# Optimization experiments

Measured on AMD Instinct MI355X. Metric: run time of the kernel, lower is better.

Reference implementation:

```python
import jax, jax.numpy as jnp
import numpy as np

B, N, M, C, T, HF, WF = 4, 512, 32, 512, 8, 14, 14
K = 80          # num_classes
P = 7           # ROI pool output size
HID = 1024
IMG = 224


def setup_inputs() -> dict:
    key = jax.random.key(0)
    k0, k1, k2, k3, k4, k5 = jax.random.split(key, 6)
    feature = jax.random.normal(k0, (B, C, T, HF, WF), dtype=jnp.float32)
    # GT boxes: realistic xyxy boxes inside a 224x224 image
    ka, kb = jax.random.split(k1)
    cxy = jax.random.uniform(ka, (B, M, 2), minval=40.0, maxval=180.0)
    wh = jax.random.uniform(kb, (B, M, 2), minval=40.0, maxval=100.0)
    gt_bboxes = jnp.concatenate([cxy - wh / 2, cxy + wh / 2], axis=-1).astype(jnp.float32)
    # Proposals: jittered copies of GT boxes so many pass the IoU>=0.85 fg test
    idx = jnp.arange(N) % M
    base = gt_bboxes[:, idx]                                   # [B,N,4]
    noise = jax.random.normal(k2, (B, N, 4), dtype=jnp.float32) * 1.5
    proposal_bboxes = jnp.clip(base + noise, 0.0, float(IMG))
    gt_classes = (jax.random.uniform(k3, (B, M, K)) < 0.1).astype(jnp.float32)
    W1 = jax.random.normal(k4, (C * P * P, HID), dtype=jnp.float32) * 0.01
    b1 = jnp.zeros((HID,), jnp.float32)
    W2 = jax.random.normal(k5, (HID, K), dtype=jnp.float32) * 0.01
    b2 = jnp.zeros((K,), jnp.float32)
    return {"feature": feature, "proposal_bboxes": proposal_bboxes,
            "gt_bboxes": gt_bboxes, "gt_classes": gt_classes,
            "W1": W1, "b1": b1, "W2": W2, "b2": b2,
            "image_h": IMG, "image_w": IMG}


def _iou(a, b):
    # a [B,N,4], b [B,M,4] xyxy -> [B,N,M]
    lt = jnp.maximum(a[:, :, None, :2], b[:, None, :, :2])
    rb = jnp.minimum(a[:, :, None, 2:], b[:, None, :, 2:])
    wh = jnp.clip(rb - lt, 0.0)
    inter = wh[..., 0] * wh[..., 1]
    area_a = (a[..., 2] - a[..., 0]) * (a[..., 3] - a[..., 1])
    area_b = (b[..., 2] - b[..., 0]) * (b[..., 3] - b[..., 1])
    return inter / (area_a[:, :, None] + area_b[:, None, :] - inter + 1e-8)


def _roi_pool(feat_bhwc, boxes, bidx, sy, sx):
    # feat_bhwc [B,H,W,C]; boxes [R,4] image coords; bilinear 7x7 ROI pooling
    H, W = feat_bhwc.shape[1], feat_bhwc.shape[2]
    x1, y1, x2, y2 = boxes[:, 0] * sx, boxes[:, 1] * sy, boxes[:, 2] * sx, boxes[:, 3] * sy
    g = (jnp.arange(P, dtype=jnp.float32) + 0.5) / P
    ys = y1[:, None] + g[None, :] * (y2 - y1)[:, None]        # [R,P]
    xs = x1[:, None] + g[None, :] * (x2 - x1)[:, None]        # [R,P]
    y = jnp.broadcast_to(ys[:, :, None], (boxes.shape[0], P, P)) - 0.5
    x = jnp.broadcast_to(xs[:, None, :], (boxes.shape[0], P, P)) - 0.5
    y0f = jnp.floor(y); x0f = jnp.floor(x)
    wy = jnp.clip(y - y0f, 0.0, 1.0)[..., None]
    wx = jnp.clip(x - x0f, 0.0, 1.0)[..., None]
    y0 = jnp.clip(y0f, 0, H - 1).astype(jnp.int32)
    y1i = jnp.clip(y0f + 1, 0, H - 1).astype(jnp.int32)
    x0 = jnp.clip(x0f, 0, W - 1).astype(jnp.int32)
    x1i = jnp.clip(x0f + 1, 0, W - 1).astype(jnp.int32)
    bi = bidx[:, None, None]
    gather = lambda yy, xx: feat_bhwc[bi, yy, xx]             # [R,P,P,C]
    out = (gather(y0, x0) * (1 - wy) * (1 - wx) + gather(y0, x1i) * (1 - wy) * wx +
           gather(y1i, x0) * wy * (1 - wx) + gather(y1i, x1i) * wy * wx)
    return out


def reference(feature, proposal_bboxes, gt_bboxes, gt_classes, W1, b1, W2, b2, image_h, image_w):
    # temporal average pool (AvgPool3d over T) -> [B,C,HF,WF]
    feat = feature.mean(axis=2)
    feat_bhwc = jnp.transpose(feat, (0, 2, 3, 1))             # [B,HF,WF,C]
    # IoU-based fg assignment
    ious = _iou(proposal_bboxes, gt_bboxes)                   # [B,N,M]
    max_iou = ious.max(axis=2)                                # [B,N]
    assign = ious.argmax(axis=2)                              # [B,N]
    any_fg = jnp.any(max_iou >= 0.85)
    thresh = jnp.where(any_fg, 0.85, 0.5)                     # fallback branch
    fg = (max_iou >= thresh).astype(feature.dtype)            # [B,N]
    # ROI pool all proposals (bg masked out in the loss)
    boxes = proposal_bboxes.reshape(B * N, 4)
    bidx = jnp.repeat(jnp.arange(B, dtype=jnp.int32), N)
    sy = feat.shape[2] / float(image_h)
    sx = feat.shape[3] / float(image_w)
    pool = _roi_pool(feat_bhwc, boxes, bidx, sy, sx)          # [R,P,P,C]
    pool = jnp.transpose(pool, (0, 3, 1, 2)).reshape(B * N, C * P * P)
    hidden = jax.nn.relu(pool @ W1 + b1)                      # [R,HID]
    logits = hidden @ W2 + b2                                 # [R,K]
    # multilabel soft-margin labels per proposal
    labels = gt_classes[jnp.repeat(jnp.arange(B), N), assign.reshape(-1)]  # [R,K]
    per = -(labels * jax.nn.log_sigmoid(logits) +
            (1.0 - labels) * jax.nn.log_sigmoid(-logits)).mean(axis=-1)    # [R]
    per = per.reshape(B, N)
    cnt = fg.sum(axis=1)
    losses = jnp.where(cnt > 0, (per * fg).sum(axis=1) / jnp.maximum(cnt, 1.0), 0.0)
    return losses
```

## Files before the change

kernel.cpp:

```cpp
#include <hip/hip_runtime.h>
#include <cstdint>
#include <cstddef>

#define KTOT 25088
#define NBOX 2048
#define HID  1024

typedef __bf16 bf16x8 __attribute__((ext_vector_type(8)));
typedef float  f32x4  __attribute__((ext_vector_type(4)));

__device__ __forceinline__ unsigned short f2bf(float f) {
  union { float f; unsigned u; } v; v.f = f;
  unsigned r = v.u + 0x7FFFu + ((v.u >> 16) & 1u);
  return (unsigned short)(r >> 16);
}

__device__ __forceinline__ float scalar_f(const void* p) {
  int iv = *(const int*)p;
  if (iv > 0 && iv < (1 << 20)) return (float)iv;
  return *(const float*)p;
}

__global__ __launch_bounds__(256) void k_meant(const float* __restrict__ feature,
                                               float* __restrict__ fbhwc) {
  int id = blockIdx.x * 256 + threadIdx.x;
  if (id >= 4 * 512 * 196) return;
  int pix = id % 196;
  int c   = (id / 196) & 511;
  int b   = id / (196 * 512);
  const float* p = feature + ((size_t)(b * 512 + c) * 8) * 196 + pix;
  float s = 0.f;
#pragma unroll
  for (int t = 0; t < 8; ++t) s += p[t * 196];
  fbhwc[((size_t)(b * 196 + pix)) * 512 + c] = s * 0.125f;
}

__global__ __launch_bounds__(256) void k_iou(const float* __restrict__ prop,
                                             const float* __restrict__ gtb,
                                             float* __restrict__ max_iou,
                                             int* __restrict__ assign,
                                             int* __restrict__ flag) {
  __shared__ float g[128];
  int gid = blockIdx.x * 256 + threadIdx.x;
  int b = gid >> 9;
  if (threadIdx.x < 128) g[threadIdx.x] = gtb[b * 128 + threadIdx.x];
  __syncthreads();
  float x1 = prop[gid * 4 + 0], y1 = prop[gid * 4 + 1];
  float x2 = prop[gid * 4 + 2], y2 = prop[gid * 4 + 3];
  float aa = (x2 - x1) * (y2 - y1);
  float best = -1e30f; int arg = 0;
  for (int m = 0; m < 32; ++m) {
    float gx1 = g[m*4], gy1 = g[m*4+1], gx2 = g[m*4+2], gy2 = g[m*4+3];
    float iw = fmaxf(fminf(x2, gx2) - fmaxf(x1, gx1), 0.f);
    float ih = fmaxf(fminf(y2, gy2) - fmaxf(y1, gy1), 0.f);
    float inter = iw * ih;
    float ab = (gx2 - gx1) * (gy2 - gy1);
    float iou = inter / (aa + ab - inter + 1e-8f);
    if (iou > best) { best = iou; arg = m; }
  }
  max_iou[gid] = best; assign[gid] = arg;
  if (best >= 0.85f) atomicOr(flag, 1);
}

__global__ __launch_bounds__(256) void k_w1t(const float* __restrict__ W1,
                                             unsigned short* __restrict__ W1T) {
  __shared__ unsigned short tile[64][68];
  int kp0 = blockIdx.x * 64;
  int h0  = blockIdx.y * 64;
  int t = threadIdx.x;
  int seg = t & 15, ro = t >> 4;
#pragma unroll
  for (int r = 0; r < 4; ++r) {
    int i = ro + r * 16;
    int kp = kp0 + i;
    int srow = (kp & 511) * 49 + (kp >> 9);
    float4 v = *(const float4*)(W1 + (size_t)srow * 1024 + h0 + seg * 4);
    tile[i][seg*4+0] = f2bf(v.x);
    tile[i][seg*4+1] = f2bf(v.y);
    tile[i][seg*4+2] = f2bf(v.z);
    tile[i][seg*4+3] = f2bf(v.w);
  }
  __syncthreads();
#pragma unroll
  for (int r = 0; r < 4; ++r) {
    int hi = ro + r * 16;
    unsigned a = tile[seg*4+0][hi];
    unsigned b = tile[seg*4+1][hi];
    unsigned c = tile[seg*4+2][hi];
    unsigned d = tile[seg*4+3][hi];
    *(uint2*)(W1T + (size_t)(h0+hi)*KTOT + kp0 + seg*4) =
        make_uint2(a | (b << 16), c | (d << 16));
  }
}

__global__ __launch_bounds__(256) void k_roipool(const float* __restrict__ fbhwc,
                                                 const float* __restrict__ prop,
                                                 const void* ihp, const void* iwp,
                                                 unsigned short* __restrict__ Apool) {
  int n = blockIdx.x;
  int tid = threadIdx.x;
  float sy = 14.f / scalar_f(ihp);
  float sx = 14.f / scalar_f(iwp);
  float bx1 = prop[n*4+0]*sx, by1 = prop[n*4+1]*sy;
  float bx2 = prop[n*4+2]*sx, by2 = prop[n*4+3]*sy;
  const float* fb = fbhwc + (size_t)(n >> 9) * 196 * 512;
  unsigned short* arow = Apool + (size_t)n * KTOT;
  int c4 = (tid & 127) << 2;
  int bh = tid >> 7;
  for (int b2i = 0; b2i < 49; b2i += 2) {
    int bin = b2i + bh;
    if (bin >= 49) continue;
    int py = bin / 7, px = bin - py * 7;
    float y = by1 + ((py + 0.5f) * (1.f/7.f)) * (by2 - by1) - 0.5f;
    float x = bx1 + ((px + 0.5f) * (1.f/7.f)) * (bx2 - bx1) - 0.5f;
    float y0f = floorf(y), x0f = floorf(x);
    float wy = y - y0f, wx = x - x0f;
    int y0  = min(max((int)y0f, 0), 13);
    int y1i = min(max((int)y0f + 1, 0), 13);
    int x0  = min(max((int)x0f, 0), 13);
    int x1i = min(max((int)x0f + 1, 0), 13);
    float w00 = (1.f - wy) * (1.f - wx), w01 = (1.f - wy) * wx;
    float w10 = wy * (1.f - wx),         w11 = wy * wx;
    const float4 f00 = *(const float4*)(fb + (y0 * 14 + x0 ) * 512 + c4);
    const float4 f01 = *(const float4*)(fb + (y0 * 14 + x1i) * 512 + c4);
    const float4 f10 = *(const float4*)(fb + (y1i * 14 + x0 ) * 512 + c4);
    const float4 f11 = *(const float4*)(fb + (y1i * 14 + x1i) * 512 + c4);
    float vx = f00.x*w00 + f01.x*w01 + f10.x*w10 + f11.x*w11;
    float vy = f00.y*w00 + f01.y*w01 + f10.y*w10 + f11.y*w11;
    float vz = f00.z*w00 + f01.z*w01 + f10.z*w10 + f11.z*w11;
    float vw = f00.w*w00 + f01.w*w01 + f10.w*w10 + f11.w*w11;
    unsigned lo = (unsigned)f2bf(vx) | ((unsigned)f2bf(vy) << 16);
    unsigned hi = (unsigned)f2bf(vz) | ((unsigned)f2bf(vw) << 16);
    *(uint2*)(arow + bin * 512 + c4) = make_uint2(lo, hi);
  }
}

__device__ __forceinline__ void gload16(const unsigned short* g, unsigned short* l) {
  __builtin_amdgcn_global_load_lds(
      (const __attribute__((address_space(1))) unsigned int*)g,
      (__attribute__((address_space(3))) unsigned int*)l, 16, 0, 0);
}

__global__ __launch_bounds__(512, 2) void k_gemm1(
    const unsigned short* __restrict__ A,
    const unsigned short* __restrict__ B,
    unsigned short* __restrict__ hp)
{
  extern __shared__ unsigned short lds[];
  const int tid  = threadIdx.x;
  const int w    = tid >> 6;
  const int lane = tid & 63;
  const int l15  = lane & 15;
  const int wr = w >> 2, wc = w & 3;
  const int bid = (int)blockIdx.x;
  const int wg  = (bid & 7) * 32 + (bid >> 3);
  const int kb  = wg >> 5;
  const int gy  = (wg >> 2) & 7;
  const int gx  = wg & 3;

  f32x4 acc[8][4];
  const f32x4 zero = {0.f, 0.f, 0.f, 0.f};
#pragma unroll
  for (int m = 0; m < 8; ++m)
#pragma unroll
    for (int n = 0; n < 4; ++n) acc[m][n] = zero;

  const int xsw  = (tid & 7) ^ ((tid >> 3) & 7);
  const int rloc = ((tid >> 3) << 1) + (xsw >> 2);
  const int qsrc = xsw & 3;
  const size_t kbase = (size_t)kb * 3136;
  const unsigned short* gAp = A + (size_t)(gy * 256 + rloc) * KTOT + kbase + qsrc * 8;
  const unsigned short* gBp = B + (size_t)(gx * 256 + rloc) * KTOT + kbase + qsrc * 8;
  const int dstc = tid * 8;

  const int pfr   = ((lane >> 4) | ((l15 & 1) << 2)) ^ (l15 >> 1);
  const int aoffc = wr * 4096 + (l15 >> 1) * 64 + pfr * 8;
  const int boffc = wc * 2048 + (l15 >> 1) * 64 + pfr * 8;

  bf16x8 af[4], bfr[4];

#define STGA(OB, KN) { \
    gload16(gAp + (KN),                      lds + (OB) + dstc); \
    gload16(gAp + (KN) + (size_t)128 * KTOT, lds + (OB) + 4096 + dstc); }
#define STGB(OB, KN) { \
    gload16(gBp + (KN),                      lds + (OB) + 8192 + dstc); \
    gload16(gBp + (KN) + (size_t)128 * KTOT, lds + (OB) + 12288 + dstc); }
#define DSRA(CB, MB) _Pragma("unroll") for (int i = 0; i < 4; ++i) \
    af[i] = *reinterpret_cast<const bf16x8*>(lds + (CB) + aoffc + ((MB) + i) * 512);
#define DSRB(CB) _Pragma("unroll") for (int n = 0; n < 4; ++n) \
    bfr[n] = *reinterpret_cast<const bf16x8*>(lds + (CB) + 8192 + boffc + n * 512);
#define MMQ(MH) _Pragma("unroll") for (int i = 0; i < 4; ++i) \
    _Pragma("unroll") for (int n = 0; n < 4; ++n) \
      acc[(MH)*4 + i][n] = __builtin_amdgcn_mfma_f32_16x16x32_bf16( \
          af[i], bfr[n], acc[(MH)*4 + i][n], 0, 0, 0);
#define PHX \
    __builtin_amdgcn_sched_barrier(0); \
    __builtin_amdgcn_s_barrier(); \
    asm volatile("s_waitcnt lgkmcnt(0)" ::: "memory"); \
    __builtin_amdgcn_sched_barrier(0); \
    __builtin_amdgcn_s_setprio(1);
#define VM4 asm volatile("s_waitcnt vmcnt(4)" ::: "memory");
#define VM0 asm volatile("s_waitcnt vmcnt(0)" ::: "memory");
#define VMN

#define KSTEP(CB, OB, KN, DOST, VME)                                          \
  {                                                   \
    DSRA(CB, 0)                                                               \
    DSRB(CB)                                                                  \
    if (DOST) STGA(OB, KN)                                                    \
    PHX  MMQ(0)                                                               \
    __builtin_amdgcn_s_setprio(0);                                            \
    __builtin_amdgcn_s_barrier();                                             \
                        \
    DSRA(CB, 4)                                                               \
    DSRB(CB)                                                                  \
    if (DOST) STGB(OB, KN)                                                    \
    PHX  MMQ(1)                                                               \
    __builtin_amdgcn_s_setprio(0);                                            \
    VME                                                                       \
    __builtin_amdgcn_s_barrier();                                             \
  }

  STGA(0, 0)      STGB(0, 0)
  STGA(16384, 32) STGB(16384, 32)
  VM4
  __builtin_amdgcn_s_barrier();

#pragma unroll 1
  for (int sq = 0; sq < 96; sq += 4) {
    const int kn = (sq + 2) * 32;
    KSTEP(0,     32768, kn,      true, VM4)
    KSTEP(16384, 49152, kn + 32, true, VM4)
    KSTEP(32768, 0,     kn + 64, true, VM4)
    KSTEP(49152, 16384, kn + 96, true, VM4)
  }
  KSTEP(0,     0, 0, false, VM0)
  KSTEP(16384, 0, 0, false, VMN)

#undef KSTEP
#undef VMN
#undef VM0
#undef VM4
#undef PHX
#undef MMQ
#undef DSRB
#undef DSRA
#undef STGB
#undef STGA

  unsigned short* o = hp + (size_t)kb * (2048u * 1024u);
  const int r0 = gy * 256 + wr * 128 + ((lane >> 4) << 2);
  const int c0 = gx * 256 + wc * 64 + l15;
#pragma unroll
  for (int m = 0; m < 8; ++m)
#pragma unroll
    for (int n = 0; n < 4; ++n)
#pragma unroll
      for (int j = 0; j < 4; ++j)
        o[(size_t)(r0 + m * 16 + j) * 1024 + c0 + n * 16] = f2bf(acc[m][n][j]);
}

template<int OUTBF>
__global__ __launch_bounds__(256, 4) void k_gemm(
    const unsigned short* __restrict__ A,
    const unsigned short* __restrict__ B,
    void* __restrict__ outp,
    int Kst, int kIters, int nTileBits, int mTileBits, int ldc)
{
  __shared__ unsigned short As[2][4096];
  __shared__ unsigned short Bs[2][4096];
  const int tid  = threadIdx.x;
  const int w    = tid >> 6;
  const int lane = tid & 63;
  const int nwg = (int)gridDim.x, cpx = nwg >> 3;
  const int bid = (int)blockIdx.x;
  const int wg  = (bid & 7) * cpx + (bid >> 3);
  const int kb  = wg >> (mTileBits + nTileBits);
  const int rem = wg & ((1 << (mTileBits + nTileBits)) - 1);
  const int gy  = rem >> nTileBits;
  const int gx  = rem & ((1 << nTileBits) - 1);
  const int wr = w >> 1, wc = w & 1;

  f32x4 acc[4][4];
  const f32x4 zero = {0.f, 0.f, 0.f, 0.f};
#pragma unroll
  for (int m = 0; m < 4; ++m)
#pragma unroll
    for (int n = 0; n < 4; ++n) acc[m][n] = zero;

  const int r0   = 32 * w + (lane >> 2);
  const int qsrc = (lane & 3) ^ ((lane >> 3) & 3);
  const size_t kbase = (size_t)kb * kIters * 32;
  const unsigned short* gA = A + (size_t)(gy * 128 + r0) * Kst + kbase + qsrc * 8;
  const unsigned short* gB = B + (size_t)(gx * 128 + r0) * Kst + kbase + qsrc * 8;
  const int ldst = r0 * 32 + (lane & 3) * 8;

  const int swq = ((lane >> 4) ^ ((lane >> 1) & 3)) * 8;
  const int ar = (wr * 64 + (lane & 15)) * 32 + swq;
  const int br = (wc * 64 + (lane & 15)) * 32 + swq;

#define STAGE(bufi, it) do {                                         \
    const unsigned short* pa = gA + (size_t)(it) * 32;               \
    const unsigned short* pb = gB + (size_t)(it) * 32;               \
    gload16(pa,                      &As[bufi][ldst]);               \
    gload16(pa + (size_t)16 * Kst,   &As[bufi][ldst + 512]);         \
    gload16(pb,                      &Bs[bufi][ldst]);               \
    gload16(pb + (size_t)16 * Kst,   &Bs[bufi][ldst + 512]);         \
  } while (0)

  STAGE(0, 0);
  int cur = 0;
  for (int kk = 0; kk < kIters; ++kk) {
    __syncthreads();
    if (kk + 1 < kIters) STAGE(cur ^ 1, kk + 1);
    bf16x8 af[4], bfr[4];
#pragma unroll
    for (int m = 0; m < 4; ++m)
      af[m] = *reinterpret_cast<const bf16x8*>(&As[cur][ar + m * 512]);
#pragma unroll
    for (int n = 0; n < 4; ++n)
      bfr[n] = *reinterpret_cast<const bf16x8*>(&Bs[cur][br + n * 512]);
#pragma unroll
    for (int m = 0; m < 4; ++m)
#pragma unroll
      for (int n = 0; n < 4; ++n)
        acc[m][n] = __builtin_amdgcn_mfma_f32_16x16x32_bf16(af[m], bfr[n], acc[m][n], 0, 0, 0);
    cur ^= 1;
  }
#undef STAGE

  const size_t M = (size_t)(1 << mTileBits) * 128;
  const size_t splitStride = M * (size_t)ldc;
  const int r0o = gy * 128 + wr * 64 + ((lane >> 4) << 2);
  const int c0o = gx * 128 + wc * 64 + (lane & 15);
  if (OUTBF) {
    unsigned short* o = (unsigned short*)outp + (size_t)kb * splitStride;
#pragma unroll
    for (int m = 0; m < 4; ++m)
#pragma unroll
      for (int n = 0; n < 4; ++n)
#pragma unroll
        for (int j = 0; j < 4; ++j)
          o[(size_t)(r0o + m * 16 + j) * ldc + c0o + n * 16] = f2bf(acc[m][n][j]);
  } else {
    float* o = (float*)outp + (size_t)kb * splitStride;
#pragma unroll
    for (int m = 0; m < 4; ++m)
#pragma unroll
      for (int n = 0; n < 4; ++n)
#pragma unroll
        for (int j = 0; j < 4; ++j)
          o[(size_t)(r0o + m * 16 + j) * ldc + c0o + n * 16] = acc[m][n][j];
  }
}

__global__ __launch_bounds__(256) void k_combine(const unsigned short* __restrict__ hp,
                                                 const float* __restrict__ b1,
                                                 unsigned short* __restrict__ hidden) {
  int gid = blockIdx.x * 256 + threadIdx.x;
  int id8 = gid * 8;
  int h = id8 & 1023;
  float a[8];
#pragma unroll
  for (int j = 0; j < 8; ++j) a[j] = b1[h + j];
#pragma unroll
  for (int s = 0; s < 8; ++s) {
    uint4 u = *(const uint4*)(hp + (size_t)s * 2097152 + id8);
    unsigned uu[4] = {u.x, u.y, u.z, u.w};
#pragma unroll
    for (int q = 0; q < 4; ++q) {
      union { unsigned u; float f; } lo, hi;
      lo.u = uu[q] << 16; hi.u = uu[q] & 0xFFFF0000u;
      a[2*q]   += lo.f;
      a[2*q+1] += hi.f;
    }
  }
  unsigned out[4];
#pragma unroll
  for (int q = 0; q < 4; ++q) {
    unsigned l  = f2bf(fmaxf(a[2*q],   0.f));
    unsigned hh = f2bf(fmaxf(a[2*q+1], 0.f));
    out[q] = l | (hh << 16);
  }
  *(uint4*)(hidden + id8) = make_uint4(out[0], out[1], out[2], out[3]);
}

__global__ __launch_bounds__(256) void k_w2t(const float* __restrict__ W2,
                                             unsigned short* __restrict__ W2T) {
  int id = blockIdx.x * 256 + threadIdx.x;
  int cls = id >> 10, k = id & 1023;
  float v = (cls < 80) ? W2[(size_t)k * 80 + cls] : 0.f;
  W2T[id] = f2bf(v);
}

__global__ __launch_bounds__(256) void k_bce(const float* __restrict__ hp2,
                                             const float* __restrict__ b2,
                                             const float* __restrict__ gtc,
                                             const int* __restrict__ assign,
                                             float* __restrict__ per) {
  __shared__ float red[256];
  int t = threadIdx.x;
  int box = t >> 4, li = t & 15;
  int n = blockIdx.x * 16 + box;
  int lab = ((n >> 9) * 32 + assign[n]) * 80;
  float s = 0.f;
#pragma unroll
  for (int j = 0; j < 5; ++j) {
    int c = li + 16 * j;
    size_t o = (size_t)n * 128 + c;
    float x = hp2[o] + hp2[o + 262144] + hp2[o + 524288] + hp2[o + 786432] + b2[c];
    float y = gtc[lab + c];
    float ce = log1pf(expf(-fabsf(x)));
    s += y * (fmaxf(-x, 0.f) + ce) + (1.f - y) * (fmaxf(x, 0.f) + ce);
  }
  red[t] = s;
  __syncthreads();
  if (li == 0) {
    float tot = 0.f;
#pragma unroll
    for (int i = 0; i < 16; ++i) tot += red[box * 16 + i];
    per[n] = tot * (1.f / 80.f);
  }
}

__global__ __launch_bounds__(512) void k_reduce(const float* __restrict__ per,
                                                const float* __restrict__ max_iou,
                                                const int* __restrict__ flag,
                                                float* __restrict__ out) {
  __shared__ float sv[8], sf[8];
  int b = blockIdx.x, tid = threadIdx.x;
  float thr = (*flag) ? 0.85f : 0.5f;
  int n = b * 512 + tid;
  float f = (max_iou[n] >= thr) ? 1.f : 0.f;
  float v = per[n] * f;
#pragma unroll
  for (int o = 32; o > 0; o >>= 1) {
    v += __shfl_down(v, o);
    f += __shfl_down(f, o);
  }
  int wv = tid >> 6;
  if ((tid & 63) == 0) { sv[wv] = v; sf[wv] = f; }
  __syncthreads();
  if (tid == 0) {
    float S = 0.f, F = 0.f;
#pragma unroll
    for (int i = 0; i < 8; ++i) { S += sv[i]; F += sf[i]; }
    out[b] = (F > 0.f) ? S / fmaxf(F, 1.f) : 0.f;
  }
}

extern "C" void kernel_launch(void* const* d_in, const int* in_sizes, int n_in,
                              void* d_out, int out_size, void* d_ws, size_t ws_size,
                              hipStream_t stream) {
  const float* feature = (const float*)d_in[0];
  const float* prop    = (const float*)d_in[1];
  const float* gtb     = (const float*)d_in[2];
  const float* gtc     = (const float*)d_in[3];
  const float* W1      = (const float*)d_in[4];
  const float* b1      = (const float*)d_in[5];
  const float* W2      = (const float*)d_in[6];
  const float* b2      = (const float*)d_in[7];
  const void*  ihp     = d_in[8];
  const void*  iwp     = d_in[9];

  char* ws = (char*)d_ws;
  float*          fbhwc  = (float*)(ws);
  unsigned short* W1T    = (unsigned short*)(ws + 1605632);
  unsigned short* Apool  = (unsigned short*)(ws + 52985856);
  unsigned short* hp     = (unsigned short*)(ws + 155746304);
  float*          max_iou= (float*)(ws + 189300736);
  int*            assign = (int*)(ws + 189308928);
  float*          per    = (float*)(ws + 189317120);
  int*            flag   = (int*)(ws + 189325312);
  unsigned short* hidden = W1T;
  unsigned short* W2T    = Apool;
  float*          hp2    = (float*)((char*)Apool + 262144);

  hipFuncSetAttribute((const void*)k_gemm1,
                      hipFuncAttributeMaxDynamicSharedMemorySize, 131072);

  hipMemsetAsync(flag, 0, sizeof(int), stream);
  k_meant  <<<1568, 256, 0, stream>>>(feature, fbhwc);
  k_iou    <<<8, 256, 0, stream>>>(prop, gtb, max_iou, assign, flag);
  k_w1t    <<<dim3(392, 16), 256, 0, stream>>>(W1, W1T);
  k_roipool<<<2048, 256, 0, stream>>>(fbhwc, prop, ihp, iwp, Apool);
  k_gemm1  <<<256, 512, 131072, stream>>>(Apool, W1T, hp);
  k_combine<<<1024, 256, 0, stream>>>(hp, b1, hidden);
  k_w2t    <<<512, 256, 0, stream>>>(W2, W2T);
  k_gemm<0><<<64, 256, 0, stream>>>(hidden, W2T, hp2, 1024, 8, 0, 4, 128);
  k_bce    <<<128, 256, 0, stream>>>(hp2, b2, gtc, assign, per);
  k_reduce <<<4, 512, 0, stream>>>(per, max_iou, flag, (float*)d_out);
}
```

Before: 203.0 us.

## Prefetch next-slot LDS fragments during MFMAs with single barrier per k-step

Restructures the split-K GEMM main loop so that all 8 A fragments and 4 B fragments for the next k-slot are loaded from LDS and interleaved with the current slot's 32 MFMAs. Each k-step now has one barrier instead of two half-steps, each of which needed two barriers. The goal is to hide LDS read latency behind matrix math and cut synchronisation. In exchange the A/B fragment registers roughly double, which adds register pressure, and it relies on the 4-slot ring keeping the next slot ready before its fragments are read.

```diff
diff --git a/kernel.cpp b/kernel.cpp
--- a/kernel.cpp
+++ b/kernel.cpp
@@ -177,76 +177,67 @@
   const int aoffc = wr * 4096 + (l15 >> 1) * 64 + pfr * 8;
   const int boffc = wc * 2048 + (l15 >> 1) * 64 + pfr * 8;
 
-  bf16x8 af[4], bfr[4];
-
-#define STGA(OB, KN) { \
-    gload16(gAp + (KN),                      lds + (OB) + dstc); \
-    gload16(gAp + (KN) + (size_t)128 * KTOT, lds + (OB) + 4096 + dstc); }
-#define STGB(OB, KN) { \
-    gload16(gBp + (KN),                      lds + (OB) + 8192 + dstc); \
-    gload16(gBp + (KN) + (size_t)128 * KTOT, lds + (OB) + 12288 + dstc); }
-#define DSRA(CB, MB) _Pragma("unroll") for (int i = 0; i < 4; ++i) \
-    af[i] = *reinterpret_cast<const bf16x8*>(lds + (CB) + aoffc + ((MB) + i) * 512);
-#define DSRB(CB) _Pragma("unroll") for (int n = 0; n < 4; ++n) \
-    bfr[n] = *reinterpret_cast<const bf16x8*>(lds + (CB) + 8192 + boffc + n * 512);
-#define MMQ(MH) _Pragma("unroll") for (int i = 0; i < 4; ++i) \
-    _Pragma("unroll") for (int n = 0; n < 4; ++n) \
-      acc[(MH)*4 + i][n] = __builtin_amdgcn_mfma_f32_16x16x32_bf16( \
-          af[i], bfr[n], acc[(MH)*4 + i][n], 0, 0, 0);
-#define PHX \
-    __builtin_amdgcn_sched_barrier(0); \
-    __builtin_amdgcn_s_barrier(); \
-    asm volatile("s_waitcnt lgkmcnt(0)" ::: "memory"); \
-    __builtin_amdgcn_sched_barrier(0); \
-    __builtin_amdgcn_s_setprio(1);
+  bf16x8 Afr[8], Bfr[4];
+
+#define STG(SLOT, KN) { \
+    gload16(gAp + (KN),                      lds + (SLOT)*16384 + dstc); \
+    gload16(gAp + (KN) + (size_t)128 * KTOT, lds + (SLOT)*16384 + 4096 + dstc); \
+    gload16(gBp + (KN),                      lds + (SLOT)*16384 + 8192 + dstc); \
+    gload16(gBp + (KN) + (size_t)128 * KTOT, lds + (SLOT)*16384 + 12288 + dstc); }
+#define LDA(i, SLOT) Afr[i] = *reinterpret_cast<const bf16x8*>( \
+    lds + (SLOT)*16384 + aoffc + (i)*512);
+#define LDB(n, SLOT) Bfr[n] = *reinterpret_cast<const bf16x8*>( \
+    lds + (SLOT)*16384 + 8192 + boffc + (n)*512);
 #define VM4 asm volatile("s_waitcnt vmcnt(4)" ::: "memory");
 #define VM0 asm volatile("s_waitcnt vmcnt(0)" ::: "memory");
 #define VMN
 
-#define KSTEP(CB, OB, KN, DOST, VME)                                          \
-  {                                                   \
-    DSRA(CB, 0)                                                               \
-    DSRB(CB)                                                                  \
-    if (DOST) STGA(OB, KN)                                                    \
-    PHX  MMQ(0)                                                               \
-    __builtin_amdgcn_s_setprio(0);                                            \
-    __builtin_amdgcn_s_barrier();                                             \
-                        \
-    DSRA(CB, 4)                                                               \
-    DSRB(CB)                                                                  \
-    if (DOST) STGB(OB, KN)                                                    \
-    PHX  MMQ(1)                                                               \
-    __builtin_amdgcn_s_setprio(0);                                            \
-    VME                                                                       \
-    __builtin_amdgcn_s_barrier();                                             \
-  }
-
-  STGA(0, 0)      STGB(0, 0)
-  STGA(16384, 32) STGB(16384, 32)
+#define STEP(CS, DOSTG, KN, VMASM, DOREFILL)                                   \
+  {                                                                            \
+    if (DOSTG) STG((((CS)+2)&3), KN)                                           \
+    VMASM                                                                      \
+    __builtin_amdgcn_s_barrier();                                              \
+    asm volatile("s_waitcnt lgkmcnt(0)" ::: "memory");                         \
+    __builtin_amdgcn_sched_barrier(0);                                         \
+    __builtin_amdgcn_s_setprio(1);                                             \
+    _Pragma("unroll") for (int i = 0; i < 8; ++i) {                            \
+      _Pragma("unroll") for (int n = 0; n < 4; ++n)                            \
+        acc[i][n] = __builtin_amdgcn_mfma_f32_16x16x32_bf16(                   \
+            Afr[i], Bfr[n], acc[i][n], 0, 0, 0);                               \
+      if (DOREFILL) LDA(i, (((CS)+1)&3))                                       \
+    }                                                                          \
+    if (DOREFILL) { _Pragma("unroll") for (int n = 0; n < 4; ++n)              \
+                      LDB(n, (((CS)+1)&3)) }                                   \
+    __builtin_amdgcn_s_setprio(0);                                             \
+    __builtin_amdgcn_sched_barrier(0);                                         \
+  }
+
+  STG(0, 0)
+  STG(1, 32)
   VM4
   __builtin_amdgcn_s_barrier();
+#pragma unroll
+  for (int i = 0; i < 8; ++i) LDA(i, 0)
+#pragma unroll
+  for (int n = 0; n < 4; ++n) LDB(n, 0)
 
 #pragma unroll 1
-  for (int sq = 0; sq < 96; sq += 4) {
-    const int kn = (sq + 2) * 32;
-    KSTEP(0,     32768, kn,      true, VM4)
-    KSTEP(16384, 49152, kn + 32, true, VM4)
-    KSTEP(32768, 0,     kn + 64, true, VM4)
-    KSTEP(49152, 16384, kn + 96, true, VM4)
-  }
-  KSTEP(0,     0, 0, false, VM0)
-  KSTEP(16384, 0, 0, false, VMN)
-
-#undef KSTEP
+  for (int s4 = 0; s4 < 96; s4 += 4) {
+    STEP(0, true, (size_t)(s4 + 2) * 32, VM4, true)
+    STEP(1, true, (size_t)(s4 + 3) * 32, VM4, true)
+    STEP(2, true, (size_t)(s4 + 4) * 32, VM4, true)
+    STEP(3, true, (size_t)(s4 + 5) * 32, VM4, true)
+  }
+  STEP(0, false, 0, VM0, true)
+  STEP(1, false, 0, VMN, false)
+
+#undef STEP
 #undef VMN
 #undef VM0
 #undef VM4
-#undef PHX
-#undef MMQ
-#undef DSRB
-#undef DSRA
-#undef STGB
-#undef STGA
+#undef LDB
+#undef LDA
+#undef STG
 
   unsigned short* o = hp + (size_t)kb * (2048u * 1024u);
   const int r0 = gy * 256 + wr * 128 + ((lane >> 4) << 2);
```

Result: no change. 200.2 us (-1.4%).
